# Optimization experiments

Measured on AMD Instinct MI355X. Metric: run time of the kernel, lower is better.

The kernel has to match this reference:

```python
import jax, jax.numpy as jnp
import numpy as np


def setup_inputs() -> dict:
    key = jax.random.key(0)
    k1, k2, k3, k4 = jax.random.split(key, 4)
    d_in, d_out, B, T = 1024, 1024, 4, 2048
    scale = 1.0 / np.sqrt(d_in)
    return {
        "x": jax.random.normal(k1, (B, T, d_in), dtype=jnp.float32),
        "Wq": jax.random.normal(k2, (d_in, d_out), dtype=jnp.float32) * scale,
        "Wk": jax.random.normal(k3, (d_in, d_out), dtype=jnp.float32) * scale,
        "Wv": jax.random.normal(k4, (d_in, d_out), dtype=jnp.float32) * scale,
    }


def reference(x, Wq, Wk, Wv):
    # x: [B, T, d_in]; Wq/Wk/Wv: [d_in, d_out] (Linear, bias=False)
    q = jnp.einsum("btd,de->bte", x, Wq)
    k = jnp.einsum("btd,de->bte", x, Wk)
    v = jnp.einsum("btd,de->bte", x, Wv)
    d_out = k.shape[-1]
    scores = jnp.einsum("bqe,bke->bqk", q, k)  # [B, T, T]
    T = x.shape[1]
    causal = jnp.triu(jnp.ones((T, T), dtype=bool), k=1)  # True above diagonal
    scores = jnp.where(causal[None, :, :], -jnp.inf, scores)
    # original divides after masking; -inf stays -inf so math is identical
    att = jax.nn.softmax(scores / jnp.sqrt(jnp.asarray(d_out, scores.dtype)), axis=-1)
    # dropout p=0.0 -> identity
    return jnp.einsum("bqk,bke->bqe", att, v)
```

## Files before the change

### kernel.cpp

```cpp
#include <hip/hip_runtime.h>
#include <stdint.h>
#include <math.h>

typedef unsigned short u16;
typedef __bf16 bf16x8 __attribute__((ext_vector_type(8)));
typedef float f32x4 __attribute__((ext_vector_type(4)));

enum { M_QKV = 0, M_SCORE = 1, M_PV = 2 };

__device__ __forceinline__ u16 f2bf(float f) {
    union { float f; unsigned int u; } a; a.f = f;
    unsigned int u = a.u;
    u += 0x7FFFu + ((u >> 16) & 1u);
    return (u16)(u >> 16);
}

__device__ __forceinline__ void async_load16(const void* g, void* l) {
    __builtin_amdgcn_global_load_lds(
        (const __attribute__((address_space(1))) void*)g,
        (__attribute__((address_space(3))) void*)l,
        16, 0, 0);
}

template<int MODE, int TBM>
__device__ __forceinline__ void gemm_core(
    const u16* __restrict__ A, const u16* __restrict__ Bt,
    void* __restrict__ Cv, float* __restrict__ rowsum,
    int bm, int bn, int bz, int M, int N, int K, float kfac,
    u16* As, u16* Bs)
{
    constexpr int KB  = 64;
    constexpr int NI  = TBM / 32;
    constexpr int ACH = TBM / 32;
    constexpr int BCH = 4;

    const int tid  = threadIdx.x;
    const int lane = tid & 63;
    const int wv   = tid >> 6;
    const int wm   = wv >> 1;
    const int wn   = wv & 1;

    f32x4 acc[NI][4] = {};

    const int rowA0 = bm * TBM, rowB0 = bn * 128;
    const int lrow  = lane >> 3;
    const int lslot = lane & 7;
    const int sg    = (lslot ^ lrow) * 8;

    int kEnd = K;
    if (MODE == M_PV) { int ke = (bm + 1) * TBM; kEnd = ke < K ? ke : K; }

    const int lm   = lane & 15;
    const int quad = lane >> 4;
    const int rx   = lm & 7;

    for (int k0 = 0; k0 < kEnd; k0 += KB) {
        #pragma unroll
        for (int c = 0; c < ACH; ++c) {
            const int cc  = wv * ACH + c;
            const int row = cc * 8 + lrow;
            async_load16(&A[(size_t)(rowA0 + row) * K + k0 + sg], &As[cc * 512 + lane * 8]);
        }
        #pragma unroll
        for (int c = 0; c < BCH; ++c) {
            const int cc  = wv * BCH + c;
            const int row = cc * 8 + lrow;
            async_load16(&Bt[(size_t)(rowB0 + row) * K + k0 + sg], &Bs[cc * 512 + lane * 8]);
        }
        __syncthreads();

        #pragma unroll
        for (int h = 0; h < 2; ++h) {
            const int sl = (((h * 4 + quad) ^ rx) * 8);
            bf16x8 af[NI], bfr[4];
            #pragma unroll
            for (int i = 0; i < NI; ++i)
                af[i] = *reinterpret_cast<const bf16x8*>(
                    &As[(wm * (TBM / 2) + i * 16 + lm) * KB + sl]);
            #pragma unroll
            for (int j = 0; j < 4; ++j)
                bfr[j] = *reinterpret_cast<const bf16x8*>(
                    &Bs[(wn * 64 + j * 16 + lm) * KB + sl]);
            #pragma unroll
            for (int i = 0; i < NI; ++i)
                #pragma unroll
                for (int j = 0; j < 4; ++j)
                    acc[i][j] = __builtin_amdgcn_mfma_f32_16x16x32_bf16(af[i], bfr[j], acc[i][j], 0, 0, 0);
        }
        __syncthreads();
    }

    if (MODE == M_QKV) {
        u16* C = (u16*)Cv + (size_t)(bn >> 3) * ((size_t)M * 1024);
        #pragma unroll
        for (int i = 0; i < NI; ++i)
            #pragma unroll
            for (int j = 0; j < 4; ++j) {
                const int r0 = rowA0 + wm * (TBM / 2) + i * 16 + quad * 4;
                const int c0 = (rowB0 + wn * 64 + j * 16 + lm) & 1023;
                #pragma unroll
                for (int g = 0; g < 4; ++g)
                    C[(size_t)(r0 + g) * 1024 + c0] = f2bf(acc[i][j][g]);
            }
    } else if (MODE == M_SCORE) {
        u16* E = (u16*)Cv + (size_t)bz * ((size_t)M * N);
        float rs[NI][4];
        #pragma unroll
        for (int i = 0; i < NI; ++i)
            #pragma unroll
            for (int g = 0; g < 4; ++g) rs[i][g] = 0.f;
        #pragma unroll
        for (int i = 0; i < NI; ++i)
            #pragma unroll
            for (int j = 0; j < 4; ++j) {
                const int r0 = rowA0 + wm * (TBM / 2) + i * 16 + quad * 4;
                const int c  = rowB0 + wn * 64 + j * 16 + lm;
                #pragma unroll
                for (int g = 0; g < 4; ++g) {
                    const int r = r0 + g;
                    float e = (c <= r) ? exp2f(acc[i][j][g] * kfac) : 0.f;
                    E[(size_t)r * N + c] = f2bf(e);
                    rs[i][g] += e;
                }
            }
        #pragma unroll
        for (int i = 0; i < NI; ++i)
            #pragma unroll
            for (int g = 0; g < 4; ++g) {
                float v = rs[i][g];
                v += __shfl_xor(v, 1); v += __shfl_xor(v, 2);
                v += __shfl_xor(v, 4); v += __shfl_xor(v, 8);
                rs[i][g] = v;
            }
        if (lm == 0) {
            #pragma unroll
            for (int i = 0; i < NI; ++i)
                #pragma unroll
                for (int g = 0; g < 4; ++g) {
                    const int r = rowA0 + wm * (TBM / 2) + i * 16 + quad * 4 + g;
                    atomicAdd(&rowsum[(size_t)bz * M + r], rs[i][g]);
                }
        }
    } else {
        float* C = (float*)Cv + (size_t)bz * ((size_t)M * N);
        #pragma unroll
        for (int i = 0; i < NI; ++i) {
            const int r0 = rowA0 + wm * (TBM / 2) + i * 16 + quad * 4;
            float inv[4];
            #pragma unroll
            for (int g = 0; g < 4; ++g)
                inv[g] = 1.f / rowsum[(size_t)bz * M + r0 + g];
            #pragma unroll
            for (int j = 0; j < 4; ++j) {
                const int c0 = rowB0 + wn * 64 + j * 16 + lm;
                #pragma unroll
                for (int g = 0; g < 4; ++g)
                    C[(size_t)(r0 + g) * N + c0] = acc[i][j][g] * inv[g];
            }
        }
    }
}

__global__ __launch_bounds__(256)
void k_qkv(const u16* __restrict__ Xb, const u16* __restrict__ Wt,
           u16* __restrict__ Q, int M, int N, int K)
{
    __shared__ __attribute__((aligned(16))) u16 As[128 * 64];
    __shared__ __attribute__((aligned(16))) u16 Bs[128 * 64];
    gemm_core<M_QKV, 128>(Xb, Wt, Q, nullptr, blockIdx.y, blockIdx.x, 0,
                          M, N, K, 0.f, As, Bs);
}

__global__ __launch_bounds__(256)
void k_score_vt(const u16* __restrict__ Q, const u16* __restrict__ Kb,
                u16* __restrict__ E, float* __restrict__ rowsum,
                const u16* __restrict__ Vb, u16* __restrict__ Vt,
                int T, int D, float kfac, int nTri)
{
    __shared__ __attribute__((aligned(16))) u16 As[128 * 64];
    __shared__ __attribute__((aligned(16))) u16 Bs[128 * 64];
    __shared__ u16 tt[32][33];
    const int bz = blockIdx.z;

    if ((int)blockIdx.x < nTri) {
        const int idx = blockIdx.x;
        int bm = (int)((sqrtf(8.f * (float)idx + 1.f) - 1.f) * 0.5f);
        while (bm * (bm + 1) / 2 > idx) --bm;
        while ((bm + 1) * (bm + 2) / 2 <= idx) ++bm;
        const int bn = idx - bm * (bm + 1) / 2;
        gemm_core<M_SCORE, 128>(Q + (size_t)bz * T * D, Kb + (size_t)bz * T * D,
                                E, rowsum, bm, bn, bz, T, T, D, kfac, As, Bs);
    } else {
        const int t  = blockIdx.x - nTri;
        const int cx = t & 31;
        const int cy = t >> 5;
        const u16* V = Vb + (size_t)bz * T * D;
        u16*      Vo = Vt + (size_t)bz * D * T;
        const int c0 = cx * 32, r0 = cy * 32;
        const int tx = threadIdx.x & 31, ty = threadIdx.x >> 5;
        #pragma unroll
        for (int s = 0; s < 32; s += 8)
            tt[ty + s][tx] = V[(size_t)(r0 + ty + s) * D + c0 + tx];
        __syncthreads();
        #pragma unroll
        for (int s = 0; s < 32; s += 8)
            Vo[(size_t)(c0 + ty + s) * T + r0 + tx] = tt[tx][ty + s];
    }
}

__global__ __launch_bounds__(256)
void k_pv(const u16* __restrict__ E, const u16* __restrict__ Vt,
          float* __restrict__ out, const float* __restrict__ rowsum,
          int T, int D)
{
    __shared__ __attribute__((aligned(16))) u16 As[128 * 64];
    __shared__ __attribute__((aligned(16))) u16 Bs[128 * 64];
    const int bz = blockIdx.z;
    const int bm = (gridDim.y - 1) - blockIdx.y;
    gemm_core<M_PV, 128>(E + (size_t)bz * T * T, Vt + (size_t)bz * D * T,
                         out, (float*)rowsum, bm, blockIdx.x, bz,
                         T, D, T, 0.f, As, Bs);
}

__global__ __launch_bounds__(256)
void k_prep(const float* __restrict__ x,
            const float* __restrict__ W0, const float* __restrict__ W1,
            const float* __restrict__ W2,
            u16* __restrict__ Xb, u16* __restrict__ Wt, float* __restrict__ RS,
            int D, int nCX, int nW)
{
    const int bx = blockIdx.x;
    if (bx < nCX) {
        long long i = ((long long)bx * 256 + threadIdx.x) * 8;
        const float4 a = *(const float4*)(x + i);
        const float4 b = *(const float4*)(x + i + 4);
        union { u16 u[8]; float4 v; } r;
        r.u[0] = f2bf(a.x); r.u[1] = f2bf(a.y); r.u[2] = f2bf(a.z); r.u[3] = f2bf(a.w);
        r.u[4] = f2bf(b.x); r.u[5] = f2bf(b.y); r.u[6] = f2bf(b.z); r.u[7] = f2bf(b.w);
        *(float4*)(Xb + i) = r.v;
    } else if (bx < nCX + nW) {
        __shared__ u16 t[32][33];
        const int w  = bx - nCX;
        const int z  = w >> 10;
        const int rm = w & 1023;
        const float* W = z == 0 ? W0 : (z == 1 ? W1 : W2);
        u16* dst = Wt + (size_t)z * D * D;
        const int c0 = (rm & 31) * 32, r0 = (rm >> 5) * 32;
        const int tx = threadIdx.x & 31, ty = threadIdx.x >> 5;
        #pragma unroll
        for (int s = 0; s < 32; s += 8)
            t[ty + s][tx] = f2bf(W[(size_t)(r0 + ty + s) * D + c0 + tx]);
        __syncthreads();
        #pragma unroll
        for (int s = 0; s < 32; s += 8)
            dst[(size_t)(c0 + ty + s) * D + r0 + tx] = t[tx][ty + s];
    } else {
        const int t = bx - nCX - nW;
        ((float4*)RS)[t * 256 + threadIdx.x] = float4{0.f, 0.f, 0.f, 0.f};
    }
}

extern "C" void kernel_launch(void* const* d_in, const int* in_sizes, int n_in,
                              void* d_out, int out_size, void* d_ws, size_t ws_size,
                              hipStream_t stream)
{
    const int B = 4, T = 2048, D = 1024;
    const float* x  = (const float*)d_in[0];
    const float* Wq = (const float*)d_in[1];
    const float* Wk = (const float*)d_in[2];
    const float* Wv = (const float*)d_in[3];
    float* out = (float*)d_out;

    const size_t nX = (size_t)B * T * D;
    u16* Xb = (u16*)d_ws;
    u16* Wt = Xb + nX;
    u16* Q  = Wt + 3 * (size_t)D * D;
    u16* Kb = Q + nX;
    u16* Vb = Kb + nX;
    u16* Vt = Vb + nX;
    char* rest = (char*)(Vt + nX);
    const size_t fixed   = (size_t)((char*)rest - (char*)d_ws);
    const size_t perb_E  = (size_t)T * T * 2;
    const size_t perb_rs = (size_t)T * 4;
    const bool full = ws_size >= fixed + (size_t)B * (perb_E + perb_rs);
    const int nb = full ? B : 1;
    u16*   E  = (u16*)rest;
    float* RS = (float*)(E + nb * (size_t)T * T);

    const float kfac = 1.4426950408889634f / 32.0f;
    const int nTri128 = 136;
    const int nCX = (int)(nX / (8 * 256));
    const int nW  = 3 * (D / 32) * (D / 32);
    const int nRS = (nb * T) / (4 * 256);

    if (full) {
        k_prep<<<dim3(nCX + nW + nRS), 256, 0, stream>>>(
            x, Wq, Wk, Wv, Xb, Wt, RS, D, nCX, nW);
        k_qkv<<<dim3(3 * D / 128, (B * T) / 128), 256, 0, stream>>>(
            Xb, Wt, Q, B * T, 3 * D, D);
        k_score_vt<<<dim3(nTri128 + (D / 32) * (T / 32), 1, B), 256, 0, stream>>>(
            Q, Kb, E, RS, Vb, Vt, T, D, kfac, nTri128);
        k_pv<<<dim3(D / 128, T / 128, B), 256, 0, stream>>>(E, Vt, out, RS, T, D);
    } else {
        k_prep<<<dim3(nCX + nW + nRS), 256, 0, stream>>>(
            x, Wq, Wk, Wv, Xb, Wt, RS, D, nCX, nW);
        k_qkv<<<dim3(3 * D / 128, (B * T) / 128), 256, 0, stream>>>(
            Xb, Wt, Q, B * T, 3 * D, D);
        for (int b = 0; b < B; ++b) {
            const size_t ob = (size_t)b * T * D;
            if (b) hipMemsetAsync(RS, 0, (size_t)T * 4, stream);
            k_score_vt<<<dim3(nTri128 + (D / 32) * (T / 32), 1, 1), 256, 0, stream>>>(
                Q + ob, Kb + ob, E, RS, Vb + ob, Vt, T, D, kfac, nTri128);
            k_pv<<<dim3(D / 128, T / 128, 1), 256, 0, stream>>>(
                E, Vt, out + ob, RS, T, D);
        }
    }
}
```

Measured before the change: 244.4 us.

## Replace QKV GEMM with 128x256-tile, 512-thread, triple-buffered async-LDS kernel

Replaces the fused QKV projection GEMM with a new kernel. Each 512-thread block computes a 128x256 output tile. K-tiles stream into a three-stage ring of swizzled LDS buffers through direct global-to-LDS async loads, with vmcnt waits so loading overlaps MFMA compute. The larger tile reuses more operand data per load and hides memory latency. The cost is 144KB of dynamic shared memory per block, which allows only one block per CU and needs a one-time attribute call, and the output indexing hardcodes a d_out of 1024.

```diff
diff --git a/kernel.cpp b/kernel.cpp
--- a/kernel.cpp
+++ b/kernel.cpp
@@ -161,14 +161,105 @@
     }
 }
 
-__global__ __launch_bounds__(256)
-void k_qkv(const u16* __restrict__ Xb, const u16* __restrict__ Wt,
-           u16* __restrict__ Q, int M, int N, int K)
-{
-    __shared__ __attribute__((aligned(16))) u16 As[128 * 64];
-    __shared__ __attribute__((aligned(16))) u16 Bs[128 * 64];
-    gemm_core<M_QKV, 128>(Xb, Wt, Q, nullptr, blockIdx.y, blockIdx.x, 0,
-                          M, N, K, 0.f, As, Bs);
+__global__ __launch_bounds__(512, 2)
+void k_qkv2(const u16* __restrict__ Xb, const u16* __restrict__ Wt,
+            u16* __restrict__ Q, int M, int N, int K)
+{
+    extern __shared__ __attribute__((aligned(16))) u16 S[];
+    const int tid  = threadIdx.x;
+    const int lane = tid & 63;
+    const int wv   = tid >> 6;
+    const int wm   = wv >> 2;
+    const int wn   = wv & 3;
+    const int bn   = blockIdx.x;
+    const int bm   = blockIdx.y;
+    const int rowA0 = bm * 128, rowB0 = bn * 256;
+
+    const int lrow  = lane >> 3;
+    const int lslot = lane & 7;
+    const int sg    = (lslot ^ lrow) * 8;
+    const int lm    = lane & 15;
+    const int quad  = lane >> 4;
+    const int rx    = lm & 7;
+
+    f32x4 acc[4][4] = {};
+
+    const int nt = K >> 6;
+
+    auto stage = [&](int t, int b) {
+        u16* As = S + b * 24576;
+        u16* Bs = As + 8192;
+        const int k0 = t << 6;
+        #pragma unroll
+        for (int c = 0; c < 2; ++c) {
+            const int cc  = wv * 2 + c;
+            const int row = cc * 8 + lrow;
+            async_load16(&Xb[(size_t)(rowA0 + row) * K + k0 + sg], &As[cc * 512 + lane * 8]);
+        }
+        #pragma unroll
+        for (int c = 0; c < 4; ++c) {
+            const int cc  = wv * 4 + c;
+            const int row = cc * 8 + lrow;
+            async_load16(&Wt[(size_t)(rowB0 + row) * K + k0 + sg], &Bs[cc * 512 + lane * 8]);
+        }
+    };
+
+    auto compute = [&](int b) {
+        const u16* As = S + b * 24576;
+        const u16* Bs = As + 8192;
+        #pragma unroll
+        for (int h = 0; h < 2; ++h) {
+            const int sl = (((h * 4 + quad) ^ rx) * 8);
+            bf16x8 af[4], bfr[4];
+            #pragma unroll
+            for (int i = 0; i < 4; ++i)
+                af[i] = *reinterpret_cast<const bf16x8*>(
+                    &As[(wm * 64 + i * 16 + lm) * 64 + sl]);
+            #pragma unroll
+            for (int j = 0; j < 4; ++j)
+                bfr[j] = *reinterpret_cast<const bf16x8*>(
+                    &Bs[(wn * 64 + j * 16 + lm) * 64 + sl]);
+            #pragma unroll
+            for (int i = 0; i < 4; ++i)
+                #pragma unroll
+                for (int j = 0; j < 4; ++j)
+                    acc[i][j] = __builtin_amdgcn_mfma_f32_16x16x32_bf16(af[i], bfr[j], acc[i][j], 0, 0, 0);
+        }
+    };
+
+    stage(0, 0);
+    stage(1, 1);
+    asm volatile("s_waitcnt vmcnt(6)" ::: "memory");
+    __builtin_amdgcn_s_barrier();
+
+    int cb = 0;
+    #pragma unroll 1
+    for (int t = 0; t < nt - 2; ++t) {
+        int sb = cb + 2; if (sb >= 3) sb -= 3;
+        stage(t + 2, sb);
+        compute(cb);
+        asm volatile("s_waitcnt vmcnt(6)" ::: "memory");
+        __builtin_amdgcn_s_barrier();
+        if (++cb == 3) cb = 0;
+    }
+    compute(cb);
+    asm volatile("s_waitcnt vmcnt(0)" ::: "memory");
+    __builtin_amdgcn_s_barrier();
+    if (++cb == 3) cb = 0;
+    compute(cb);
+
+    u16* C = Q + (size_t)(bn >> 2) * ((size_t)M * 1024);
+    const int cbase = (rowB0 & 1023) + wn * 64;
+    #pragma unroll
+    for (int i = 0; i < 4; ++i)
+        #pragma unroll
+        for (int j = 0; j < 4; ++j) {
+            const int r0 = rowA0 + wm * 64 + i * 16 + quad * 4;
+            const int c0 = cbase + j * 16 + lm;
+            #pragma unroll
+            for (int g = 0; g < 4; ++g)
+                C[(size_t)(r0 + g) * 1024 + c0] = f2bf(acc[i][j][g]);
+        }
 }
 
 __global__ __launch_bounds__(256)
@@ -293,10 +384,18 @@
     const int nW  = 3 * (D / 32) * (D / 32);
     const int nRS = (nb * T) / (4 * 256);
 
+    static bool attr_done = false;
+    if (!attr_done) {
+        (void)hipFuncSetAttribute((const void*)k_qkv2,
+                                  hipFuncAttributeMaxDynamicSharedMemorySize,
+                                  147456);
+        attr_done = true;
+    }
+
     if (full) {
         k_prep<<<dim3(nCX + nW + nRS), 256, 0, stream>>>(
             x, Wq, Wk, Wv, Xb, Wt, RS, D, nCX, nW);
-        k_qkv<<<dim3(3 * D / 128, (B * T) / 128), 256, 0, stream>>>(
+        k_qkv2<<<dim3(3 * D / 256, (B * T) / 128), 512, 147456, stream>>>(
             Xb, Wt, Q, B * T, 3 * D, D);
         k_score_vt<<<dim3(nTri128 + (D / 32) * (T / 32), 1, B), 256, 0, stream>>>(
             Q, Kb, E, RS, Vb, Vt, T, D, kfac, nTri128);
@@ -304,7 +403,7 @@
     } else {
         k_prep<<<dim3(nCX + nW + nRS), 256, 0, stream>>>(
             x, Wq, Wk, Wv, Xb, Wt, RS, D, nCX, nW);
-        k_qkv<<<dim3(3 * D / 128, (B * T) / 128), 256, 0, stream>>>(
+        k_qkv2<<<dim3(3 * D / 256, (B * T) / 128), 512, 147456, stream>>>(
             Xb, Wt, Q, B * T, 3 * D, D);
         for (int b = 0; b < B; ++b) {
             const size_t ob = (size_t)b * T * D;
```

Result: no change. 244.4 us (-0.0%).
